# Kernel optimization log

Measured on AMD Instinct MI355X. Metric: run time of the kernel, lower is better.

Reference implementation:

```python
import jax, jax.numpy as jnp
import numpy as np

SIGMA = 1.0
KSIZE = 5
WEAK = 75.0
STRONG = 255.0
LOW_T = 0.00392
HIGH_T = 0.15

# scipy.signal.gaussian(M, std): unnormalized gaussian window
_n = np.arange(KSIZE, dtype=np.float32) - (KSIZE - 1) / 2.0
_g = np.exp(-0.5 * (_n / SIGMA) ** 2).astype(np.float32)
GAUSS_H = jnp.asarray(_g.reshape(1, 1, 1, KSIZE))  # horizontal 1xK
GAUSS_V = jnp.asarray(_g.reshape(1, 1, KSIZE, 1))  # vertical Kx1

_sobel = np.array([[1, 0, -1], [2, 0, -2], [1, 0, -1]], dtype=np.float32)
SOBEL_H = jnp.asarray(_sobel.reshape(1, 1, 3, 3))
SOBEL_V = jnp.asarray(_sobel.T.reshape(1, 1, 3, 3))

_f0 = np.array([[0, 0, 0], [0, 1, -1], [0, 0, 0]], np.float32)
_f45 = np.array([[0, 0, 0], [0, 1, 0], [0, 0, -1]], np.float32)
_f90 = np.array([[0, 0, 0], [0, 1, 0], [0, -1, 0]], np.float32)
_f135 = np.array([[0, 0, 0], [0, 1, 0], [-1, 0, 0]], np.float32)
_f180 = np.array([[0, 0, 0], [-1, 1, 0], [0, 0, 0]], np.float32)
_f225 = np.array([[-1, 0, 0], [0, 1, 0], [0, 0, 0]], np.float32)
_f270 = np.array([[0, -1, 0], [0, 1, 0], [0, 0, 0]], np.float32)
_f315 = np.array([[0, 0, -1], [0, 1, 0], [0, 0, 0]], np.float32)
DIR_FILT = jnp.asarray(np.stack([_f0, _f45, _f90, _f135, _f180, _f225, _f270, _f315]).reshape(8, 1, 3, 3))

NBR_FILT = jnp.asarray(np.array([[1, 1, 1], [1, 0, 1], [1, 1, 1]], np.float32).reshape(1, 1, 3, 3))


def _conv(x, w, pad):
    # cross-correlation, matching torch F.conv2d
    return jax.lax.conv_general_dilated(
        x, w, window_strides=(1, 1), padding=[(pad[0], pad[0]), (pad[1], pad[1])],
        dimension_numbers=('NCHW', 'OIHW', 'NCHW'))


def setup_inputs() -> dict:
    key = jax.random.key(0)
    img = jax.random.uniform(key, (16, 1, 1024, 1024), dtype=jnp.float32)
    return {"img": img}


def reference(img):
    B = img.shape[0]
    # --- gaussian noise removal (separable) ---
    sm = _conv(img, GAUSS_H, (0, KSIZE // 2))
    sm = _conv(sm, GAUSS_V, (KSIZE // 2, 0))
    # --- sobel gradients ---
    Ix = _conv(sm, SOBEL_H, (1, 1))
    Iy = _conv(sm, SOBEL_V, (1, 1))
    mag = jnp.sqrt(Ix ** 2 + Iy ** 2)
    mag = mag / mag.reshape(B, -1).max(axis=1).reshape(B, 1, 1, 1)
    direction = jnp.arctan2(Iy, Ix) * (180.0 / 3.1415926) + 180.0
    direction = jnp.round(direction / 45.0) * 45.0
    # --- non-max suppression via directional differences + gather ---
    all_filtered = _conv(mag, DIR_FILT, (1, 1))  # [B,8,H,W]
    idx_pos = (direction / 45.0).astype(jnp.int32) % 8  # [B,1,H,W]
    idx_neg = (idx_pos + 4) % 8
    cs_pos = jnp.take_along_axis(all_filtered, idx_pos, axis=1)
    cs_neg = jnp.take_along_axis(all_filtered, idx_neg, axis=1)
    is_max = jnp.minimum(cs_pos, cs_neg) > 0.0
    thin = jnp.where(is_max, mag, 0.0)
    # --- double threshold ---
    hi = thin.max() * HIGH_T  # global max, as in source
    strong = thin >= hi
    weak = (thin < hi) & (thin >= LOW_T)
    inter = jnp.where(strong, STRONG, jnp.where(weak, WEAK, 0.0))
    # --- hysteresis: iterate until no weak pixel gains a strong neighbor ---
    def cond(state):
        return state[1]

    def body(state):
        x, _ = state
        weak_m = x == WEAK
        sn = _conv((x == STRONG).astype(jnp.float32), NBR_FILT, (1, 1))
        new_strong = weak_m & (sn > 0.0)
        x = jnp.where(new_strong, STRONG, x)
        return x, new_strong.any()

    final, _ = jax.lax.while_loop(cond, body, (inter, jnp.asarray(True)))
    final = jnp.where(final == STRONG, final, 0.0)
    return final
```

## Files before the change

### kernel.cpp

```cpp
#include <hip/hip_runtime.h>
#include <math.h>

#define BB 16
#define H 1024
#define W 1024
#define HW (H*W)
#define NTOT (BB*HW)
#define CAP 262144u

typedef unsigned long long u64;

__device__ __constant__ float GW[5] = {
    0.13533528323661270f, 0.60653065971263342f, 1.0f,
    0.60653065971263342f, 0.13533528323661270f};

__device__ __constant__ int NBDY[8] = {0, 1, 1, 1, 0, -1, -1, -1};
__device__ __constant__ int NBDX[8] = {1, 1, 0, -1, -1, -1, 0, 1};

#define CSCALE ((float)(180.0 / 3.1415926))

__global__ __launch_bounds__(256, 6) void k_smooth_sobel_nms(
    const float* __restrict__ img, float* __restrict__ thin,
    float* __restrict__ partialA, float* __restrict__ partialB,
    unsigned int* __restrict__ cnt, uint4* __restrict__ list) {
#pragma clang fp contract(off)
    __shared__ float sA[2200];
    __shared__ float sB[24 * 76];
    unsigned short* sBk = (unsigned short*)&sA[2016];
    float* redS = &sA[2178];

    const int tid = threadIdx.x;
    const int x0 = blockIdx.x * 64;
    const int y0 = blockIdx.y * 16;
    const int b = blockIdx.z;
    const size_t base = (size_t)b * HW;

    for (int idx = tid; idx < 24 * 20; idx += 256) {
        int r = idx / 20, v = idx - r * 20;
        int gy = y0 - 4 + r;
        int gxv = x0 - 8 + v * 4;
        float4 val = make_float4(0.f, 0.f, 0.f, 0.f);
        if (gy >= 0 && gy < H && gxv >= 0 && gxv <= W - 4)
            val = *(const float4*)&img[base + (size_t)gy * W + gxv];
        *(float4*)&sA[r * 84 + v * 4] = val;
    }
    __syncthreads();

    for (int idx = tid; idx < 24 * 19; idx += 256) {
        int r = idx / 19, g = idx - r * 19;
        const float* p = &sA[r * 84 + g * 4];
        float4 A0 = *(const float4*)p;
        float4 A1 = *(const float4*)(p + 4);
        float a_[8] = {A0.x, A0.y, A0.z, A0.w, A1.x, A1.y, A1.z, A1.w};
        float o[4];
#pragma unroll
        for (int j = 0; j < 4; ++j) {
            float s = 0.0f;
#pragma unroll
            for (int k = 0; k < 5; ++k) s = s + GW[k] * a_[j + k];
            o[j] = s;
        }
        *(float4*)&sB[r * 76 + g * 4] = make_float4(o[0], o[1], o[2], o[3]);
    }
    __syncthreads();

    for (int idx = tid; idx < 20 * 19; idx += 256) {
        int rr = idx / 19, g = idx - rr * 19;
        float bb[20];
#pragma unroll
        for (int k = 0; k < 5; ++k) {
            float4 t = *(const float4*)&sB[(rr + k) * 76 + g * 4];
            bb[k * 4 + 0] = t.x; bb[k * 4 + 1] = t.y;
            bb[k * 4 + 2] = t.z; bb[k * 4 + 3] = t.w;
        }
        int gy = y0 - 2 + rr;
        bool rowok = (gy >= 0 && gy < H);
        float o[4];
#pragma unroll
        for (int j = 0; j < 4; ++j) {
            float s = 0.0f;
#pragma unroll
            for (int k = 0; k < 5; ++k) s = s + GW[k] * bb[k * 4 + j];
            int gx = x0 - 6 + g * 4 + j;
            o[j] = (rowok && gx >= 0 && gx < W) ? s : 0.0f;
        }
        *(float4*)&sA[rr * 84 + g * 4] = make_float4(o[0], o[1], o[2], o[3]);
    }
    __syncthreads();

    for (int idx = tid; idx < 18 * 18; idx += 256) {
        int m = idx / 18, gq = idx - m * 18;
        const float* P0 = &sA[m * 84 + gq * 4];
        const float* P1 = P0 + 84;
        const float* P2 = P1 + 84;
        float4 q0 = *(const float4*)P0; float4 e0 = *(const float4*)(P0 + 4);
        float4 q1 = *(const float4*)P1; float4 e1 = *(const float4*)(P1 + 4);
        float4 q2 = *(const float4*)P2; float4 e2 = *(const float4*)(P2 + 4);
        float r0[8] = {q0.x, q0.y, q0.z, q0.w, e0.x, e0.y, e0.z, e0.w};
        float r1[8] = {q1.x, q1.y, q1.z, q1.w, e1.x, e1.y, e1.z, e1.w};
        float r2[8] = {q2.x, q2.y, q2.z, q2.w, e2.x, e2.y, e2.z, e2.w};
        int gy = y0 - 1 + m;
        unsigned int bk = 0;
        float mg[4];
#pragma unroll
        for (int j = 0; j < 4; ++j) {
            float a00 = r0[j + 1], a01 = r0[j + 2], a02 = r0[j + 3];
            float a10 = r1[j + 1],                  a12 = r1[j + 3];
            float a20 = r2[j + 1], a21 = r2[j + 2], a22 = r2[j + 3];

            float Ix = a00;
            Ix = Ix - a02;
            Ix = Ix + 2.0f * a10;
            Ix = Ix - 2.0f * a12;
            Ix = Ix + a20;
            Ix = Ix - a22;

            float Iy = a00;
            Iy = Iy + 2.0f * a01;
            Iy = Iy + a02;
            Iy = Iy - a20;
            Iy = Iy - 2.0f * a21;
            Iy = Iy - a22;

            float t1 = Ix * Ix;
            float t2 = Iy * Iy;
            float m2 = sqrtf(t1 + t2);
            int gx = x0 - 4 + gq * 4 + j;
            if (gy < 0 || gy >= H || gx < 0 || gx >= W) m2 = 0.0f;
            mg[j] = m2;

            float ax = fabsf(Ix), ay = fabsf(Iy);
            float mn = fminf(ax, ay), mx = fmaxf(ax, ay);
            float cr = mn * 0.92387953f - mx * 0.38268343f;
            int bidx;
            if (fabsf(cr) < mx * 3e-5f) {
                float fa2 = (float)atan2((double)Iy, (double)Ix);
                float d2 = fa2 * CSCALE;
                d2 = d2 + 180.0f;
                float t2d = d2 / 45.0f;
                float rr2 = rintf(t2d);
                bidx = ((int)rr2) & 7;
            } else if (ay <= ax * 0.41421356f) {
                bidx = signbit(Ix) ? 0 : 4;
            } else if (ay >= ax * 2.41421356f) {
                bidx = (Iy >= 0.0f) ? 6 : 2;
            } else {
                bidx = (Iy >= 0.0f) ? ((Ix >= 0.0f) ? 5 : 7)
                                    : ((Ix >= 0.0f) ? 3 : 1);
            }
            bk |= ((unsigned int)bidx) << (4 * j);
        }
        *(float4*)&sB[m * 76 + gq * 4] = make_float4(mg[0], mg[1], mg[2], mg[3]);
        sBk[m * 18 + gq] = (unsigned short)bk;
    }
    __syncthreads();

    const int r = tid >> 4;
    const int cg = (tid & 15) * 4;
    const int y = y0 + r;
    const int m = r + 1;
    float tmax = 0.0f, amax = 0.0f;
    {
        unsigned int bk4 = sBk[m * 18 + (cg >> 2) + 1];
        float4 a4 = *(const float4*)&sB[m * 76 + cg + 4];
        float av[4] = {a4.x, a4.y, a4.z, a4.w};
        float o[4];
#pragma unroll
        for (int j = 0; j < 4; ++j) {
            int bkt = (bk4 >> (4 * j)) & 7;
            int dy = NBDY[bkt], dx = NBDX[bkt];
            int cm = cg + 4 + j;
            float a = av[j];
            float bp = sB[(m + dy) * 76 + cm + dx];
            float bn = sB[(m - dy) * 76 + cm - dx];
            bool g1 = a > bp, g2 = a > bn;
            bool im = g1 && g2;
            if (im) {
                bool f1 = a >= bp * 1.0000005f;
                bool f2 = a >= bn * 1.0000005f;
                if (!(f1 && f2)) {
                    im = false;
                    unsigned int id = atomicAdd(cnt, 1u);
                    if (id < CAP) {
                        uint4 e;
                        e.x = (unsigned int)(base + (size_t)y * W + x0 + cg + j);
                        e.y = __float_as_uint(a);
                        e.z = __float_as_uint(bp);
                        e.w = __float_as_uint(bn);
                        list[id] = e;
                    }
                }
            }
            tmax = fmaxf(tmax, a);
            if (im) amax = fmaxf(amax, a);
            o[j] = im ? a : 0.0f;
        }
        *(float4*)&thin[base + (size_t)y * W + x0 + cg] =
            make_float4(o[0], o[1], o[2], o[3]);
    }
#pragma unroll
    for (int off = 32; off > 0; off >>= 1) {
        tmax = fmaxf(tmax, __shfl_down(tmax, off));
        amax = fmaxf(amax, __shfl_down(amax, off));
    }
    if ((tid & 63) == 0) { redS[tid >> 6] = tmax; redS[4 + (tid >> 6)] = amax; }
    __syncthreads();
    if (tid == 0) {
        float tA = fmaxf(fmaxf(redS[0], redS[1]), fmaxf(redS[2], redS[3]));
        float tB = fmaxf(fmaxf(redS[4], redS[5]), fmaxf(redS[6], redS[7]));
        int pb = (b * 64 + blockIdx.y) * 16 + blockIdx.x;
        partialA[pb] = tA;
        partialB[pb] = tB;
    }
}

__global__ __launch_bounds__(1024) void k_post(const float* __restrict__ partialA,
                                               const float* __restrict__ partialB,
                                               const unsigned int* __restrict__ cnt,
                                               const uint4* __restrict__ list,
                                               float* __restrict__ thin,
                                               float* __restrict__ hdr,
                                               float* __restrict__ thr) {
#pragma clang fp contract(off)
    __shared__ float sM[16];
    __shared__ int sAmaxI[16];
    __shared__ float sTm[16];
    __shared__ float sTmAll;
    const int tid = threadIdx.x;
    const int iw = tid >> 6, lane = tid & 63;

    {
        const float* p = partialA + iw * 1024;
        float m = 0.0f;
        for (int k = lane; k < 1024; k += 64) m = fmaxf(m, p[k]);
        for (int off = 32; off > 0; off >>= 1) m = fmaxf(m, __shfl_down(m, off));
        if (lane == 0) { sM[iw] = m; sAmaxI[iw] = 0; hdr[iw] = m; }
    }
    __syncthreads();

    {
        unsigned int n = *cnt;
        if (n > CAP) n = CAP;
        for (unsigned int i = tid; i < n; i += 1024) {
            uint4 e = list[i];
            float a = __uint_as_float(e.y);
            float bp = __uint_as_float(e.z);
            float bn = __uint_as_float(e.w);
            int b = (int)(e.x >> 20);
            float M = sM[b];
            bool f1 = a >= bp * 1.0000005f;
            bool f2 = a >= bn * 1.0000005f;
            float qa = a / M;
            bool r1 = f1 ? true : (qa > (bp / M));
            bool r2 = f2 ? true : (qa > (bn / M));
            if (r1 && r2) {
                thin[e.x] = a;
                atomicMax(&sAmaxI[b], __float_as_int(a));
            }
        }
    }
    __syncthreads();

    {
        const float* p = partialB + iw * 1024;
        float m = 0.0f;
        for (int k = lane; k < 1024; k += 64) m = fmaxf(m, p[k]);
        for (int off = 32; off > 0; off >>= 1) m = fmaxf(m, __shfl_down(m, off));
        if (lane == 0) {
            m = fmaxf(m, __int_as_float(sAmaxI[iw]));
            sTm[iw] = m / sM[iw];
        }
    }
    __syncthreads();
    if (tid == 0) {
        float tm = 0.0f;
        for (int i = 0; i < 16; ++i) tm = fmaxf(tm, sTm[i]);
        hdr[16] = tm;
        sTmAll = tm;
    }
    __syncthreads();
    if (tid < 32) {
        float tm = sTmAll;
        int t = tid;
        float M = sM[t >> 1];
        float T = (t & 1) ? (tm * 0.15f) : 0.00392f;
        if (0.0f / M >= T) { thr[t] = 0.0f; return; }
        unsigned int lo = 0u, hi = 0x7f800000u;
        while (hi - lo > 1u) {
            unsigned int mid = lo + ((hi - lo) >> 1);
            if (__uint_as_float(mid) / M >= T) hi = mid; else lo = mid;
        }
        thr[t] = __uint_as_float(hi);
    }
}

__global__ __launch_bounds__(256, 8) void k_thresh_b(const float* __restrict__ thin,
                                                     const float* __restrict__ hdr,
                                                     const float* __restrict__ thr,
                                                     u64* __restrict__ Sb,
                                                     u64* __restrict__ Wb) {
    __shared__ unsigned int nibS[256], nibW[256];
    const int tid = threadIdx.x;
    const int x0 = blockIdx.x * 128;
    const int y0 = blockIdx.y * 32;
    const int b = blockIdx.z;
    const size_t base = (size_t)b * HW;
    const float Alo = thr[b * 2], Ahi = thr[b * 2 + 1];
    const bool snm = (hdr[16] * 0.15f <= 0.0f);
    const int r = tid >> 5;
    const int cg = (tid & 31) * 4;

    for (int k4 = 0; k4 < 4; ++k4) {
        const int rr = k4 * 8 + r;
        const int y = y0 + rr;
        float4 a4 = *(const float4*)&thin[base + (size_t)y * W + x0 + cg];
        float av[4] = {a4.x, a4.y, a4.z, a4.w};
        unsigned int ns = 0, nw = 0;
#pragma unroll
        for (int j = 0; j < 4; ++j) {
            bool strong = snm || (av[j] >= Ahi);
            bool weak = (!strong) && (av[j] >= Alo);
            ns |= (strong ? 1u : 0u) << j;
            nw |= (weak ? 1u : 0u) << j;
        }
        nibS[tid] = ns;
        nibW[tid] = nw;
        __syncthreads();
        if (tid < 32) {
            bool isW = (tid >= 16);
            int t = tid & 15;
            int rw = t >> 1, h = t & 1;
            const unsigned int* nb = isW ? nibW : nibS;
            u64 w = 0;
#pragma unroll
            for (int j = 0; j < 16; ++j)
                w |= (u64)nb[rw * 32 + h * 16 + j] << (4 * j);
            int yy = y0 + k4 * 8 + rw;
            int widx2 = ((b << 8) | ((yy >> 6) << 4) | ((x0 >> 6) + h)) * 64 + (yy & 63);
            if (isW) Wb[widx2] = w; else Sb[widx2] = w;
        }
        __syncthreads();
    }
}

template <bool LAST>
__global__ __launch_bounds__(256) void k_hyster_bits(const u64* __restrict__ Wb,
                                                     u64* __restrict__ Sb,
                                                     float* __restrict__ out) {
    const int lane = threadIdx.x & 63;
    const int t = blockIdx.x * 4 + (threadIdx.x >> 6);
    const int ty = (t >> 4) & 15;
    const int tx = t & 15;
    const int idx = t * 64 + lane;

    u64 S = Sb[idx];
    const u64 Wk = Wb[idx];

    u64 hstat = 0;
    if (tx > 0)  hstat |= (Sb[(t - 1) * 64 + lane] >> 63) & 1ull;
    if (tx < 15) hstat |= (Sb[(t + 1) * 64 + lane] & 1ull) << 63;

    u64 halo = 0;
    if (lane == 0 && ty > 0) {
        const int ta = t - 16;
        u64 tc = Sb[ta * 64 + 63];
        u64 hh = (tc << 1) | tc | (tc >> 1);
        if (tx > 0)  hh |= (Sb[(ta - 1) * 64 + 63] >> 63) & 1ull;
        if (tx < 15) hh |= (Sb[(ta + 1) * 64 + 63] & 1ull) << 63;
        halo = hh;
    }
    if (lane == 63 && ty < 15) {
        const int tb = t + 16;
        u64 tc = Sb[tb * 64 + 0];
        u64 hh = (tc << 1) | tc | (tc >> 1);
        if (tx > 0)  hh |= (Sb[(tb - 1) * 64 + 0] >> 63) & 1ull;
        if (tx < 15) hh |= (Sb[(tb + 1) * 64 + 0] & 1ull) << 63;
        halo = hh;
    }

    {
        u64 eu = __shfl_up(hstat, 1, 64);
        u64 ed = __shfl_down(hstat, 1, 64);
        if (lane == 0)  eu = halo;
        if (lane == 63) ed = halo;
        S |= Wk & (hstat | eu | ed);
    }

    for (int it = 0; it < 160; ++it) {
        u64 x = S;
        x |= (x << 1) & Wk;
        x |= (x >> 1) & Wk;
        u64 pL = Wk & (Wk << 1);
        u64 pR = Wk & (Wk >> 1);
        x |= (x << 2) & pL;   x |= (x >> 2) & pR;
        pL &= pL << 2;        pR &= pR >> 2;
        x |= (x << 4) & pL;   x |= (x >> 4) & pR;
        pL &= pL << 4;        pR &= pR >> 4;
        x |= (x << 8) & pL;   x |= (x >> 8) & pR;
        pL &= pL << 8;        pR &= pR >> 8;
        x |= (x << 16) & pL;  x |= (x >> 16) & pR;
        pL &= pL << 16;       pR &= pR >> 16;
        x |= (x << 32) & pL;  x |= (x >> 32) & pR;
        u64 hh = x | (x << 1) | (x >> 1);
        u64 up = __shfl_up(hh, 1, 64);
        if (lane == 0) up = 0;
        u64 dn = __shfl_down(hh, 1, 64);
        if (lane == 63) dn = 0;
        u64 nS = x | (Wk & (up | dn));
        bool ch = (nS != S);
        S = nS;
        if (!__any(ch)) break;
    }

    if (!LAST) {
        Sb[idx] = S;
    } else {
        const int bimg = t >> 8;
        float* op = out + (size_t)bimg * HW + (size_t)(ty * 64) * W + tx * 64 + lane;
#pragma unroll 4
        for (int rr = 0; rr < 64; ++rr) {
            u64 wrow = __shfl(S, rr, 64);
            op[(size_t)rr * W] = ((wrow >> lane) & 1ull) ? 255.0f : 0.0f;
        }
    }
}

extern "C" void kernel_launch(void* const* d_in, const int* in_sizes, int n_in,
                              void* d_out, int out_size, void* d_ws, size_t ws_size,
                              hipStream_t stream) {
    (void)in_sizes; (void)n_in; (void)out_size; (void)ws_size;
    const float* img = (const float*)d_in[0];
    float* out = (float*)d_out;

    float* hdr = (float*)d_ws;
    float* thr = hdr + 64;
    unsigned int* cnt = (unsigned int*)(hdr + 96);
    float* partialA = hdr + 128;
    float* partialB = partialA + 16384;
    uint4* list = (uint4*)(partialB + 16384);
    float* thin = (float*)((char*)list + (size_t)CAP * 16);
    u64* Sb = (u64*)(thin + (size_t)NTOT);
    u64* Wb = Sb + NTOT / 64;

    hipMemsetAsync(cnt, 0, sizeof(unsigned int), stream);

    dim3 blk(256);
    k_smooth_sobel_nms<<<dim3(16, 64, BB), blk, 0, stream>>>(img, thin, partialA,
                                                             partialB, cnt, list);
    k_post<<<dim3(1), dim3(1024), 0, stream>>>(partialA, partialB, cnt, list,
                                               thin, hdr, thr);
    k_thresh_b<<<dim3(8, 32, BB), blk, 0, stream>>>(thin, hdr, thr, Sb, Wb);
    for (int p = 0; p < 5; ++p)
        k_hyster_bits<false><<<dim3(NTOT / (64 * 64) / 4), blk, 0, stream>>>(Wb, Sb, out);
    k_hyster_bits<true><<<dim3(NTOT / (64 * 64) / 4), blk, 0, stream>>>(Wb, Sb, out);
}
```

Measured before the change: 262.3 us.

## Add vertical log-step propagation to hysteresis loop and shrink shared tile stride

Within each hysteresis iteration, the strong-edge mask is now propagated vertically through runs of weak pixels using log-step warp shuffles up and down. Before, each iteration advanced only one row vertically. This should reduce the number of loop iterations needed to converge. Separately, the shared-memory row stride in the smoothing/Sobel kernel drops from 84 to 80 floats, the scratch offsets are moved, and the min-blocks launch bound is removed. The narrower stride may change LDS bank conflicts, and dropping the launch bound changes register allocation and occupancy. The extra shuffles add per-iteration cost, and the scratch arrays now alias rows of sA, so correctness depends on those rows not being live at the same time.

```diff
diff --git a/kernel.cpp b/kernel.cpp
--- a/kernel.cpp
+++ b/kernel.cpp
@@ -19,15 +19,15 @@
 
 #define CSCALE ((float)(180.0 / 3.1415926))
 
-__global__ __launch_bounds__(256, 6) void k_smooth_sobel_nms(
+__global__ __launch_bounds__(256) void k_smooth_sobel_nms(
     const float* __restrict__ img, float* __restrict__ thin,
     float* __restrict__ partialA, float* __restrict__ partialB,
     unsigned int* __restrict__ cnt, uint4* __restrict__ list) {
 #pragma clang fp contract(off)
-    __shared__ float sA[2200];
+    __shared__ float sA[24 * 80];
     __shared__ float sB[24 * 76];
-    unsigned short* sBk = (unsigned short*)&sA[2016];
-    float* redS = &sA[2178];
+    unsigned short* sBk = (unsigned short*)&sA[1600];
+    float* redS = &sA[1800];
 
     const int tid = threadIdx.x;
     const int x0 = blockIdx.x * 64;
@@ -42,13 +42,13 @@
         float4 val = make_float4(0.f, 0.f, 0.f, 0.f);
         if (gy >= 0 && gy < H && gxv >= 0 && gxv <= W - 4)
             val = *(const float4*)&img[base + (size_t)gy * W + gxv];
-        *(float4*)&sA[r * 84 + v * 4] = val;
+        *(float4*)&sA[r * 80 + v * 4] = val;
     }
     __syncthreads();
 
     for (int idx = tid; idx < 24 * 19; idx += 256) {
         int r = idx / 19, g = idx - r * 19;
-        const float* p = &sA[r * 84 + g * 4];
+        const float* p = &sA[r * 80 + g * 4];
         float4 A0 = *(const float4*)p;
         float4 A1 = *(const float4*)(p + 4);
         float a_[8] = {A0.x, A0.y, A0.z, A0.w, A1.x, A1.y, A1.z, A1.w};
@@ -84,15 +84,15 @@
             int gx = x0 - 6 + g * 4 + j;
             o[j] = (rowok && gx >= 0 && gx < W) ? s : 0.0f;
         }
-        *(float4*)&sA[rr * 84 + g * 4] = make_float4(o[0], o[1], o[2], o[3]);
+        *(float4*)&sA[rr * 80 + g * 4] = make_float4(o[0], o[1], o[2], o[3]);
     }
     __syncthreads();
 
     for (int idx = tid; idx < 18 * 18; idx += 256) {
         int m = idx / 18, gq = idx - m * 18;
-        const float* P0 = &sA[m * 84 + gq * 4];
-        const float* P1 = P0 + 84;
-        const float* P2 = P1 + 84;
+        const float* P0 = &sA[m * 80 + gq * 4];
+        const float* P1 = P0 + 80;
+        const float* P2 = P1 + 80;
         float4 q0 = *(const float4*)P0; float4 e0 = *(const float4*)(P0 + 4);
         float4 q1 = *(const float4*)P1; float4 e1 = *(const float4*)(P1 + 4);
         float4 q2 = *(const float4*)P2; float4 e2 = *(const float4*)(P2 + 4);
@@ -406,9 +406,37 @@
         if (lane == 0) up = 0;
         u64 dn = __shfl_down(hh, 1, 64);
         if (lane == 63) dn = 0;
-        u64 nS = x | (Wk & (up | dn));
-        bool ch = (nS != S);
-        S = nS;
+        u64 y = x | (Wk & (up | dn));
+        {
+            u64 P = Wk;
+            y |= __shfl_up(y, 1, 64) & P;
+            u64 P2 = P & __shfl_up(P, 1, 64);
+            y |= __shfl_up(y, 2, 64) & P2;
+            u64 P4 = P2 & __shfl_up(P2, 2, 64);
+            y |= __shfl_up(y, 4, 64) & P4;
+            u64 P8 = P4 & __shfl_up(P4, 4, 64);
+            y |= __shfl_up(y, 8, 64) & P8;
+            u64 P16 = P8 & __shfl_up(P8, 8, 64);
+            y |= __shfl_up(y, 16, 64) & P16;
+            u64 P32 = P16 & __shfl_up(P16, 16, 64);
+            y |= __shfl_up(y, 32, 64) & P32;
+        }
+        {
+            u64 P = Wk;
+            y |= __shfl_down(y, 1, 64) & P;
+            u64 P2 = P & __shfl_down(P, 1, 64);
+            y |= __shfl_down(y, 2, 64) & P2;
+            u64 P4 = P2 & __shfl_down(P2, 2, 64);
+            y |= __shfl_down(y, 4, 64) & P4;
+            u64 P8 = P4 & __shfl_down(P4, 4, 64);
+            y |= __shfl_down(y, 8, 64) & P8;
+            u64 P16 = P8 & __shfl_down(P8, 8, 64);
+            y |= __shfl_down(y, 16, 64) & P16;
+            u64 P32 = P16 & __shfl_down(P16, 16, 64);
+            y |= __shfl_down(y, 32, 64) & P32;
+        }
+        bool ch = (y != S);
+        S = y;
         if (!__any(ch)) break;
     }
 
```

Measured after the change: 285.3 us. 8.8% more time.
